# Performance work log

Measured on AMD Instinct MI355X. Metric: run time of the kernel, lower is better.

The kernel has to match this reference:

```python
import jax, jax.numpy as jnp
import numpy as np
import math

N = 50000      # nodes
E = 800000     # edges (avg degree 16)
T = 4          # time steps
F = 64         # feature dim (in = hidden = out)
MAX_LEN = 200  # positional encoding table length
EPS = 1e-5     # BatchNorm eps


def _make_pe(time_dim, max_len):
    pe = np.zeros((max_len, time_dim), dtype=np.float32)
    position = np.arange(max_len, dtype=np.float32)[:, None]
    div_term = np.exp(np.arange(0, time_dim, 2, dtype=np.float32) * (-math.log(10000.0) / time_dim))
    pe[:, 0::2] = np.sin(position * div_term)
    pe[:, 1::2] = np.cos(position * div_term)
    return jnp.asarray(pe)


def setup_inputs() -> dict:
    key = jax.random.key(0)
    ks = jax.random.split(key, 10)
    xav = math.sqrt(2.0 / (F + F))  # xavier_normal_ std for square linear
    return {
        "node_features": jax.random.normal(ks[0], (N, T, F), dtype=jnp.float32),
        "edges_weight": jax.random.uniform(ks[1], (T, E), dtype=jnp.float32),
        "identities": jax.random.randint(ks[2], (T,), 0, MAX_LEN),
        "edge_src": jax.random.randint(ks[3], (E,), 0, N),
        "edge_dst": jax.random.randint(ks[4], (E,), 0, N),
        "pe": _make_pe(F, MAX_LEN),
        "W0": jax.random.normal(ks[5], (F, F), dtype=jnp.float32) * xav,
        "W1": jax.random.normal(ks[6], (F, F), dtype=jnp.float32) * xav,
        "g0": jnp.ones((F,), jnp.float32),
        "b0": jnp.zeros((F,), jnp.float32),
        "g1": jnp.ones((F,), jnp.float32),
        "b1": jnp.zeros((F,), jnp.float32),
    }


def _gcn_layer(h, ew, edge_src, edge_dst, W):
    # gather-mul-scatter: msg_e = h[src_e] * w_e ; agg_v = sum_{e: dst=v} msg_e
    msg = h[edge_src] * ew                                   # (E, T, F)
    agg = jax.ops.segment_sum(msg, edge_dst, num_segments=N)  # (N, T, F)
    readout = agg.mean(axis=0)                                # dgl.mean_nodes (single graph) -> (T, F)
    return agg @ W, readout @ W


def _batchnorm(x, gamma, beta):
    # training-mode batch stats over all non-channel dims
    mean = x.mean(axis=(0, 1))
    var = x.var(axis=(0, 1))
    return (x - mean) * jax.lax.rsqrt(var + EPS) * gamma + beta


def reference(node_features, edges_weight, identities, edge_src, edge_dst,
              pe, W0, W1, g0, b0, g1, b1):
    # positional encoding added per time step
    h = node_features + pe[identities]          # (N, T, F)
    ew = edges_weight.T[:, :, None]             # (E, T, 1)
    # layer 0: gcn -> dropout(eval=identity) -> BN -> ReLU
    h, readout = _gcn_layer(h, ew, edge_src, edge_dst, W0)
    h = jax.nn.relu(_batchnorm(h, g0, b0))
    # layer 1 (output layer)
    h, readout = _gcn_layer(h, ew, edge_src, edge_dst, W1)
    h = jax.nn.relu(_batchnorm(h, g1, b1))
    return h, readout
```

## Files before the change

kernel.cpp:

```cpp
#include <hip/hip_runtime.h>

#define TF 256

typedef __attribute__((ext_vector_type(8))) short short8;
typedef __attribute__((ext_vector_type(4))) float f32x4;
typedef __attribute__((ext_vector_type(4))) unsigned int uint4v;
typedef __attribute__((ext_vector_type(2))) unsigned int uint2v;

__device__ inline unsigned short f2bf(float x) {
  unsigned u = __float_as_uint(x);
  u += 0x7fffu + ((u >> 16) & 1u);
  return (unsigned short)(u >> 16);
}
__device__ inline unsigned pack2(unsigned short lo, unsigned short hi) {
  return (unsigned)lo | ((unsigned)hi << 16);
}
__device__ inline float bflo(unsigned u) { return __uint_as_float(u << 16); }
__device__ inline float bfhi(unsigned u) { return __uint_as_float(u & 0xffff0000u); }

__global__ void prep_hist_kernel(const float* __restrict__ x, const float* __restrict__ pe,
                                 const int* __restrict__ ids, uint2v* __restrict__ h0, int n4,
                                 const int* __restrict__ dst, int* __restrict__ indeg, int E) {
  const int gid = blockIdx.x * blockDim.x + threadIdx.x;
  const int stride = gridDim.x * blockDim.x;
  for (int i = gid; i < n4; i += stride) {
    int e0 = (i << 2) & (TF - 1);
    int t = e0 >> 6;
    int f4 = e0 & 63;
    f32x4 v = __builtin_nontemporal_load(&reinterpret_cast<const f32x4*>(x)[i]);
    const f32x4 p = *reinterpret_cast<const f32x4*>(&pe[ids[t] * 64 + f4]);
    uint2v o;
    o.x = pack2(f2bf(v.x + p.x), f2bf(v.y + p.y));
    o.y = pack2(f2bf(v.z + p.z), f2bf(v.w + p.w));
    h0[i] = o;
  }
  for (int e = gid; e < E; e += stride) {
    atomicAdd(&indeg[__builtin_nontemporal_load(&dst[e])], 1);
  }
}

__global__ __launch_bounds__(1024) void scan_part1(const int* __restrict__ indeg,
                                                   int* __restrict__ partials, int n) {
  __shared__ int wsum[16];
  const int tid = threadIdx.x;
  const int lane = tid & 63;
  const int wid = tid >> 6;
  int i = blockIdx.x * 1024 + tid;
  int s = (i < n) ? indeg[i] : 0;
  #pragma unroll
  for (int o = 1; o < 64; o <<= 1) s += __shfl_xor(s, o, 64);
  if (lane == 0) wsum[wid] = s;
  __syncthreads();
  if (tid == 0) {
    int acc = 0;
    #pragma unroll
    for (int w = 0; w < 16; ++w) acc += wsum[w];
    partials[blockIdx.x] = acc;
  }
}

__global__ __launch_bounds__(512) void scan2_wfrag_kernel(
    const int* __restrict__ partials, int* __restrict__ base, int* __restrict__ offsets,
    int nb, int n, const float* __restrict__ W0, const float* __restrict__ W1,
    short* __restrict__ wf0, short* __restrict__ wf1) {
  const int tid = threadIdx.x;
  if (tid < 64) {
    int v = (tid < nb) ? partials[tid] : 0;
    int s = v;
    #pragma unroll
    for (int o = 1; o < 64; o <<= 1) {
      int t = __shfl_up(s, o, 64);
      if (tid >= o) s += t;
    }
    if (tid < nb) base[tid] = s - v;
    if (tid == nb - 1) offsets[n] = s;
  }
  const int frag = tid >> 6, lane = tid & 63;
  const int c = frag >> 1, h = frag & 1;
  const int col = (c << 4) + (lane & 15);
  const int k0 = h * 32 + ((lane >> 4) << 3);
  short* o0 = wf0 + frag * 512 + lane * 8;
  short* o1 = wf1 + frag * 512 + lane * 8;
  #pragma unroll
  for (int i = 0; i < 8; ++i) {
    o0[i] = (short)f2bf(W0[(k0 + i) * 64 + col]);
    o1[i] = (short)f2bf(W1[(k0 + i) * 64 + col]);
  }
}

__global__ __launch_bounds__(1024) void scan_part3(const int* __restrict__ indeg,
                                                   const int* __restrict__ base,
                                                   int* __restrict__ offsets, int n) {
  __shared__ int wsum[16];
  const int tid = threadIdx.x;
  const int lane = tid & 63;
  const int wid = tid >> 6;
  int i = blockIdx.x * 1024 + tid;
  int v = (i < n) ? indeg[i] : 0;
  int s = v;
  #pragma unroll
  for (int o = 1; o < 64; o <<= 1) {
    int t = __shfl_up(s, o, 64);
    if (lane >= o) s += t;
  }
  if (lane == 63) wsum[wid] = s;
  __syncthreads();
  if (tid == 0) {
    int acc = 0;
    #pragma unroll
    for (int w = 0; w < 16; ++w) { int t = wsum[w]; wsum[w] = acc; acc += t; }
  }
  __syncthreads();
  int excl = s - v + wsum[wid] + base[blockIdx.x];
  if (i < n) offsets[i] = excl;
}

__global__ __launch_bounds__(256) void binscatter_kernel(
    const int* __restrict__ src, const int* __restrict__ dst,
    const float* __restrict__ ew, int* __restrict__ gbin_cursor,
    uint4v* __restrict__ tmp, int E, int nbins) {
  __shared__ int hist[256];
  __shared__ int hist2[256];
  __shared__ int basearr[256];
  const int tid = threadIdx.x;
  hist[tid] = 0;
  hist2[tid] = 0;
  __syncthreads();
  const int epb = (E + gridDim.x - 1) / gridDim.x;
  const int beg = blockIdx.x * epb;
  const int end = min(beg + epb, E);
  for (int e = beg + tid; e < end; e += 256)
    atomicAdd(&hist[__builtin_nontemporal_load(&dst[e]) >> 8], 1);
  __syncthreads();
  if (tid < nbins && hist[tid] > 0)
    basearr[tid] = atomicAdd(&gbin_cursor[tid], hist[tid]);
  __syncthreads();
  for (int e = beg + tid; e < end; e += 256) {
    const int d = dst[e];
    const int bin = d >> 8;
    const int idx = atomicAdd(&hist2[bin], 1);
    uint4v ent;
    ent.x = (unsigned)(src[e] << 9);
    ent.y = pack2(f2bf(ew[e]), f2bf(ew[(size_t)E + e]));
    ent.z = pack2(f2bf(ew[2 * (size_t)E + e]), f2bf(ew[3 * (size_t)E + e]));
    ent.w = (unsigned)d;
    const int pos = basearr[bin] + idx;
    if (pos < 8192)
      __builtin_nontemporal_store(ent, &tmp[((size_t)bin << 13) + pos]);
  }
}

__global__ __launch_bounds__(256) void csr_build_kernel(
    const uint4v* __restrict__ tmp, const int* __restrict__ gbin_cursor,
    const int* __restrict__ offsets, uint4v* __restrict__ csr_ent, int n) {
  __shared__ int cur[256];
  const int bin = blockIdx.x;
  const int tid = threadIdx.x;
  const int node = (bin << 8) + tid;
  cur[tid] = (node < n) ? offsets[node] : 0;
  __syncthreads();
  int cnt = gbin_cursor[bin];
  if (cnt > 8192) cnt = 8192;
  const uint4v* bt = tmp + ((size_t)bin << 13);
  for (int i = tid; i < cnt; i += 256) {
    uint4v ent = __builtin_nontemporal_load(&bt[i]);
    const int local = (int)(ent.w & 255u);
    const int pos = atomicAdd(&cur[local], 1);
    ent.w = 0u;
    __builtin_nontemporal_store(ent, &csr_ent[pos]);
  }
}

template <int LAYER>
__global__ __launch_bounds__(256, 6) void fused_agg_mm_kernel(
    const char* __restrict__ h_base, const int* __restrict__ offsets,
    const uint4v* __restrict__ csr_ent, const short* __restrict__ wf,
    const float* __restrict__ red, const float* __restrict__ g,
    const float* __restrict__ b, float inv_count,
    unsigned short* __restrict__ y_bf, float* __restrict__ part, int n_groups) {
  __shared__ unsigned short tile[2][16][72];
  __shared__ float s_sc[64], s_sh[64];
  const int tid = threadIdx.x;
  const int lane = tid & 63;
  const int wid = tid >> 6;
  if (LAYER == 1) {
    if (tid < 64) {
      float sum = red[tid] + red[64 + tid] + red[128 + tid] + red[192 + tid];
      float mean = sum * inv_count;
      float var = red[256 + tid] * inv_count - mean * mean;
      float sc = g[tid] * rsqrtf(var + 1e-5f);
      s_sc[tid] = sc;
      s_sh[tid] = fmaf(-mean, sc, b[tid]);
    }
    __syncthreads();
  }
  const short8 bf0 = *reinterpret_cast<const short8*>(wf + (wid * 2 + 0) * 512 + lane * 8);
  const short8 bf1 = *reinterpret_cast<const short8*>(wf + (wid * 2 + 1) * 512 + lane * 8);

  const int p = lane >> 5;
  const unsigned q = lane & 31;
  const unsigned qb = q << 4;
  const int tw = q >> 3;

  float scv[8], shv[8];
  if (LAYER == 1) {
    const int f0 = (q & 7) << 3;
    #pragma unroll
    for (int j = 0; j < 8; ++j) { scv[j] = s_sc[f0 + j]; shv[j] = s_sh[f0 + j]; }
  }

  f32x4 csum = (f32x4){0.f, 0.f, 0.f, 0.f};
  float ssq = 0.f;
  int buf = 0;

  for (int grp = blockIdx.x; grp < n_groups; grp += gridDim.x) {
    const int v = grp * 4 + wid;
    float acc[8];
    #pragma unroll
    for (int j = 0; j < 8; ++j) acc[j] = 0.f;

    auto wext = [&](uint4v ent) -> float {
      unsigned word = (tw & 2) ? ent.z : ent.y;
      return (tw & 1) ? bfhi(word) : bflo(word);
    };
    auto body = [&](uint4v u, float w) {
      float x[8] = {bflo(u.x), bfhi(u.x), bflo(u.y), bfhi(u.y),
                    bflo(u.z), bfhi(u.z), bflo(u.w), bfhi(u.w)};
      #pragma unroll
      for (int j = 0; j < 8; ++j) {
        float t = x[j];
        if (LAYER == 1) t = fmaxf(0.f, fmaf(t, scv[j], shv[j]));
        acc[j] = fmaf(w, t, acc[j]);
      }
    };

    const int beg = offsets[v];
    const int end = offsets[v + 1];
    int i = beg;
    for (; i + 8 <= end; i += 8) {
      uint4v ent[4];
      #pragma unroll
      for (int c = 0; c < 4; ++c) ent[c] = csr_ent[i + 2 * c + p];
      uint4v row[4];
      #pragma unroll
      for (int c = 0; c < 4; ++c)
        row[c] = *reinterpret_cast<const uint4v*>(h_base + (ent[c].x + qb));
      #pragma unroll
      for (int c = 0; c < 4; ++c) body(row[c], wext(ent[c]));
    }
    for (; i + 2 <= end; i += 2) {
      const uint4v ent = csr_ent[i + p];
      const uint4v row = *reinterpret_cast<const uint4v*>(h_base + (ent.x + qb));
      body(row, wext(ent));
    }
    if (i < end) {
      const uint4v ent = csr_ent[i];
      const uint4v row = *reinterpret_cast<const uint4v*>(h_base + (ent.x + qb));
      body(row, p == 0 ? wext(ent) : 0.f);
    }

    #pragma unroll
    for (int j = 0; j < 8; ++j) acc[j] += __shfl_xor(acc[j], 32, 64);
    if (lane < 32) {
      uint4v o;
      o.x = pack2(f2bf(acc[0]), f2bf(acc[1]));
      o.y = pack2(f2bf(acc[2]), f2bf(acc[3]));
      o.z = pack2(f2bf(acc[4]), f2bf(acc[5]));
      o.w = pack2(f2bf(acc[6]), f2bf(acc[7]));
      *reinterpret_cast<uint4v*>(&tile[buf][wid * 4 + (q >> 3)][(q & 7) * 8]) = o;
    }
    __syncthreads();

    const int r = lane & 15;
    const int k0 = (lane >> 4) << 3;
    const short8 a0 = *reinterpret_cast<const short8*>(&tile[buf][r][k0]);
    const short8 a1 = *reinterpret_cast<const short8*>(&tile[buf][r][k0 + 32]);
    f32x4 dacc = (f32x4){0.f, 0.f, 0.f, 0.f};
    dacc = __builtin_amdgcn_mfma_f32_16x16x32_bf16(a0, bf0, dacc, 0, 0, 0);
    dacc = __builtin_amdgcn_mfma_f32_16x16x32_bf16(a1, bf1, dacc, 0, 0, 0);
    const int gbase = grp * 16 + ((lane >> 4) << 2);
    const int col = (wid << 4) + (lane & 15);
    #pragma unroll
    for (int i2 = 0; i2 < 4; ++i2) {
      const float val = dacc[i2];
      y_bf[(size_t)(gbase + i2) * 64 + col] = f2bf(val);
      csum[i2] += val;
      ssq += val * val;
    }
    buf ^= 1;
  }

  #pragma unroll
  for (int i2 = 0; i2 < 4; ++i2) {
    float vv = csum[i2];
    vv += __shfl_xor(vv, 16, 64);
    vv += __shfl_xor(vv, 32, 64);
    csum[i2] = vv;
  }
  float qq = ssq;
  qq += __shfl_xor(qq, 16, 64);
  qq += __shfl_xor(qq, 32, 64);
  if (lane < 16) {
    #pragma unroll
    for (int i2 = 0; i2 < 4; ++i2)
      part[(size_t)blockIdx.x * 320 + i2 * 64 + (wid << 4) + lane] = csum[i2];
    part[(size_t)blockIdx.x * 320 + 256 + (wid << 4) + lane] = qq;
  }
}

__global__ __launch_bounds__(1024) void reduce_part_kernel(const float* __restrict__ part,
                                                           float* __restrict__ red, int nblk) {
  __shared__ float lds[1024];
  const int tid = threadIdx.x;
  const int col = blockIdx.x * 16 + (tid & 15);
  const int r = tid >> 4;
  float s = 0.f;
  for (int bk = r; bk < nblk; bk += 64) s += part[(size_t)bk * 320 + col];
  lds[tid] = s;
  __syncthreads();
  #pragma unroll
  for (int off = 512; off >= 16; off >>= 1) {
    if (tid < off) lds[tid] += lds[tid + off];
    __syncthreads();
  }
  if (tid < 16) red[col] = lds[tid];
}

__global__ __launch_bounds__(256) void bn_relu_out_kernel(
    const uint4v* __restrict__ yb, const float* __restrict__ red,
    const float* __restrict__ g, const float* __restrict__ b, float inv_count,
    float* __restrict__ out_readout, float invN, f32x4* __restrict__ out, int n8) {
  __shared__ float s_sc[64], s_sh[64];
  const int tid = threadIdx.x;
  if (tid < 64) {
    float sum = red[tid] + red[64 + tid] + red[128 + tid] + red[192 + tid];
    float mean = sum * inv_count;
    float var = red[256 + tid] * inv_count - mean * mean;
    float sc = g[tid] * rsqrtf(var + 1e-5f);
    s_sc[tid] = sc;
    s_sh[tid] = fmaf(-mean, sc, b[tid]);
  }
  __syncthreads();
  if (blockIdx.x == 0) out_readout[tid] = red[tid] * invN;
  const int i = blockIdx.x * 256 + tid;
  if (i >= n8) return;
  const int f0 = (i & 7) << 3;
  uint4v u = __builtin_nontemporal_load(&yb[i]);
  float x[8] = {bflo(u.x), bfhi(u.x), bflo(u.y), bfhi(u.y),
                bflo(u.z), bfhi(u.z), bflo(u.w), bfhi(u.w)};
  f32x4 o0, o1;
  o0.x = fmaxf(0.f, fmaf(x[0], s_sc[f0 + 0], s_sh[f0 + 0]));
  o0.y = fmaxf(0.f, fmaf(x[1], s_sc[f0 + 1], s_sh[f0 + 1]));
  o0.z = fmaxf(0.f, fmaf(x[2], s_sc[f0 + 2], s_sh[f0 + 2]));
  o0.w = fmaxf(0.f, fmaf(x[3], s_sc[f0 + 3], s_sh[f0 + 3]));
  o1.x = fmaxf(0.f, fmaf(x[4], s_sc[f0 + 4], s_sh[f0 + 4]));
  o1.y = fmaxf(0.f, fmaf(x[5], s_sc[f0 + 5], s_sh[f0 + 5]));
  o1.z = fmaxf(0.f, fmaf(x[6], s_sc[f0 + 6], s_sh[f0 + 6]));
  o1.w = fmaxf(0.f, fmaf(x[7], s_sc[f0 + 7], s_sh[f0 + 7]));
  __builtin_nontemporal_store(o0, &out[i * 2 + 0]);
  __builtin_nontemporal_store(o1, &out[i * 2 + 1]);
}

extern "C" void kernel_launch(void* const* d_in, const int* in_sizes, int n_in,
                              void* d_out, int out_size, void* d_ws, size_t ws_size,
                              hipStream_t stream) {
  const float* node_features = (const float*)d_in[0];
  const float* edges_weight  = (const float*)d_in[1];
  const int*   identities    = (const int*)d_in[2];
  const int*   edge_src      = (const int*)d_in[3];
  const int*   edge_dst      = (const int*)d_in[4];
  const float* pe            = (const float*)d_in[5];
  const float* W0            = (const float*)d_in[6];
  const float* W1            = (const float*)d_in[7];
  const float* g0            = (const float*)d_in[8];
  const float* b0            = (const float*)d_in[9];
  const float* g1            = (const float*)d_in[10];
  const float* b1            = (const float*)d_in[11];

  const int T = in_sizes[2];
  const int E = in_sizes[3];
  const int F = in_sizes[8];
  const int N = in_sizes[0] / (T * F);
  const int R = N * T;
  const int nbins = (N + 255) >> 8;

  float* out = (float*)d_out;
  float* out_h = out;
  float* out_readout = out + (size_t)N * T * F;

  char* ws = (char*)d_ws;
  size_t off = 0;
  auto alloc = [&](size_t bytes) -> void* {
    off = (off + 255) & ~(size_t)255;
    void* p = ws + off;
    off += bytes;
    return p;
  };
  int* zeros = (int*)alloc(((size_t)N + 256) * sizeof(int));
  int* indeg = zeros;
  int* gbin_cursor = zeros + N;
  int*    partials = (int*)alloc(64 * sizeof(int));
  int*    base_    = (int*)alloc(64 * sizeof(int));
  int*    offsets  = (int*)alloc(((size_t)N + 1) * sizeof(int));
  uint4v* csr_ent  = (uint4v*)alloc(((size_t)E + 16) * 16);
  uint4v* tmp      = (uint4v*)alloc(((size_t)nbins << 13) * 16);
  unsigned short* h0b  = (unsigned short*)alloc((size_t)N * TF * 2);
  unsigned short* y0b  = (unsigned short*)alloc((size_t)N * TF * 2);
  short* wf0 = (short*)alloc(8 * 512 * sizeof(short));
  short* wf1 = (short*)alloc(8 * 512 * sizeof(short));
  const int FB = 1536;
  float* mm_part = (float*)alloc((size_t)FB * 320 * sizeof(float));
  float* red     = (float*)alloc(320 * sizeof(float));
  (void)ws_size;

  const int nb = (N + 1023) / 1024;
  const float invR = 1.0f / (float)R;
  const int n_groups = N / 4;

  (void)hipMemsetAsync(zeros, 0, ((size_t)N + 256) * sizeof(int), stream);
  hipLaunchKernelGGL(prep_hist_kernel, dim3(2048), dim3(256), 0, stream,
                     node_features, pe, identities, (uint2v*)h0b, (N * TF) / 4,
                     edge_dst, indeg, E);
  hipLaunchKernelGGL(binscatter_kernel, dim3(256), dim3(256), 0, stream,
                     edge_src, edge_dst, edges_weight, gbin_cursor, tmp, E, nbins);
  hipLaunchKernelGGL(scan_part1, dim3(nb), dim3(1024), 0, stream, indeg, partials, N);
  hipLaunchKernelGGL(scan2_wfrag_kernel, dim3(1), dim3(512), 0, stream,
                     partials, base_, offsets, nb, N, W0, W1, wf0, wf1);
  hipLaunchKernelGGL(scan_part3, dim3(nb), dim3(1024), 0, stream, indeg, base_, offsets, N);
  hipLaunchKernelGGL(csr_build_kernel, dim3(nbins), dim3(256), 0, stream,
                     tmp, gbin_cursor, offsets, csr_ent, N);

  hipLaunchKernelGGL((fused_agg_mm_kernel<0>), dim3(FB), dim3(256), 0, stream,
                     (const char*)h0b, offsets, csr_ent, wf0,
                     nullptr, nullptr, nullptr, 0.f, y0b, mm_part, n_groups);
  hipLaunchKernelGGL(reduce_part_kernel, dim3(20), dim3(1024), 0, stream, mm_part, red, FB);

  hipLaunchKernelGGL((fused_agg_mm_kernel<1>), dim3(FB), dim3(256), 0, stream,
                     (const char*)y0b, offsets, csr_ent, wf1,
                     red, g0, b0, invR, h0b , mm_part, n_groups);
  hipLaunchKernelGGL(reduce_part_kernel, dim3(20), dim3(1024), 0, stream, mm_part, red, FB);

  hipLaunchKernelGGL(bn_relu_out_kernel, dim3((R * 8 + 255) / 256), dim3(256), 0, stream,
                     (const uint4v*)h0b, red, g1, b1, invR,
                     out_readout, 1.0f / (float)N, (f32x4*)out_h, R * 8);
}
```

Measured before the change: 285.1 us.

## Derive CSR offsets inside per-bin build, dropping global degree histogram and scans

```diff
diff --git a/kernel.cpp b/kernel.cpp
--- a/kernel.cpp
+++ b/kernel.cpp
@@ -18,10 +18,12 @@
 __device__ inline float bflo(unsigned u) { return __uint_as_float(u << 16); }
 __device__ inline float bfhi(unsigned u) { return __uint_as_float(u & 0xffff0000u); }
 
-__global__ void prep_hist_kernel(const float* __restrict__ x, const float* __restrict__ pe,
-                                 const int* __restrict__ ids, uint2v* __restrict__ h0, int n4,
-                                 const int* __restrict__ dst, int* __restrict__ indeg, int E) {
-  const int gid = blockIdx.x * blockDim.x + threadIdx.x;
+__global__ void prep_kernel(const float* __restrict__ x, const float* __restrict__ pe,
+                            const int* __restrict__ ids, uint2v* __restrict__ h0, int n4,
+                            const float* __restrict__ W0, const float* __restrict__ W1,
+                            short* __restrict__ wf0, short* __restrict__ wf1) {
+  const int tid = threadIdx.x;
+  const int gid = blockIdx.x * blockDim.x + tid;
   const int stride = gridDim.x * blockDim.x;
   for (int i = gid; i < n4; i += stride) {
     int e0 = (i << 2) & (TF - 1);
@@ -34,85 +36,23 @@
     o.y = pack2(f2bf(v.z + p.z), f2bf(v.w + p.w));
     h0[i] = o;
   }
-  for (int e = gid; e < E; e += stride) {
-    atomicAdd(&indeg[__builtin_nontemporal_load(&dst[e])], 1);
-  }
-}
-
-__global__ __launch_bounds__(1024) void scan_part1(const int* __restrict__ indeg,
-                                                   int* __restrict__ partials, int n) {
-  __shared__ int wsum[16];
-  const int tid = threadIdx.x;
-  const int lane = tid & 63;
-  const int wid = tid >> 6;
-  int i = blockIdx.x * 1024 + tid;
-  int s = (i < n) ? indeg[i] : 0;
-  #pragma unroll
-  for (int o = 1; o < 64; o <<= 1) s += __shfl_xor(s, o, 64);
-  if (lane == 0) wsum[wid] = s;
-  __syncthreads();
-  if (tid == 0) {
-    int acc = 0;
-    #pragma unroll
-    for (int w = 0; w < 16; ++w) acc += wsum[w];
-    partials[blockIdx.x] = acc;
-  }
-}
-
-__global__ __launch_bounds__(512) void scan2_wfrag_kernel(
-    const int* __restrict__ partials, int* __restrict__ base, int* __restrict__ offsets,
-    int nb, int n, const float* __restrict__ W0, const float* __restrict__ W1,
-    short* __restrict__ wf0, short* __restrict__ wf1) {
-  const int tid = threadIdx.x;
-  if (tid < 64) {
-    int v = (tid < nb) ? partials[tid] : 0;
-    int s = v;
-    #pragma unroll
-    for (int o = 1; o < 64; o <<= 1) {
-      int t = __shfl_up(s, o, 64);
-      if (tid >= o) s += t;
-    }
-    if (tid < nb) base[tid] = s - v;
-    if (tid == nb - 1) offsets[n] = s;
-  }
-  const int frag = tid >> 6, lane = tid & 63;
-  const int c = frag >> 1, h = frag & 1;
-  const int col = (c << 4) + (lane & 15);
-  const int k0 = h * 32 + ((lane >> 4) << 3);
-  short* o0 = wf0 + frag * 512 + lane * 8;
-  short* o1 = wf1 + frag * 512 + lane * 8;
-  #pragma unroll
-  for (int i = 0; i < 8; ++i) {
-    o0[i] = (short)f2bf(W0[(k0 + i) * 64 + col]);
-    o1[i] = (short)f2bf(W1[(k0 + i) * 64 + col]);
-  }
-}
-
-__global__ __launch_bounds__(1024) void scan_part3(const int* __restrict__ indeg,
-                                                   const int* __restrict__ base,
-                                                   int* __restrict__ offsets, int n) {
-  __shared__ int wsum[16];
-  const int tid = threadIdx.x;
-  const int lane = tid & 63;
-  const int wid = tid >> 6;
-  int i = blockIdx.x * 1024 + tid;
-  int v = (i < n) ? indeg[i] : 0;
-  int s = v;
-  #pragma unroll
-  for (int o = 1; o < 64; o <<= 1) {
-    int t = __shfl_up(s, o, 64);
-    if (lane >= o) s += t;
-  }
-  if (lane == 63) wsum[wid] = s;
-  __syncthreads();
-  if (tid == 0) {
-    int acc = 0;
-    #pragma unroll
-    for (int w = 0; w < 16; ++w) { int t = wsum[w]; wsum[w] = acc; acc += t; }
-  }
-  __syncthreads();
-  int excl = s - v + wsum[wid] + base[blockIdx.x];
-  if (i < n) offsets[i] = excl;
+  if (blockIdx.x == gridDim.x - 1) {
+    const int lane = tid & 63;
+    #pragma unroll
+    for (int fi = 0; fi < 2; ++fi) {
+      const int frag = (tid >> 6) + fi * 4;
+      const int c = frag >> 1, h = frag & 1;
+      const int col = (c << 4) + (lane & 15);
+      const int k0 = h * 32 + ((lane >> 4) << 3);
+      short* o0 = wf0 + frag * 512 + lane * 8;
+      short* o1 = wf1 + frag * 512 + lane * 8;
+      #pragma unroll
+      for (int i = 0; i < 8; ++i) {
+        o0[i] = (short)f2bf(W0[(k0 + i) * 64 + col]);
+        o1[i] = (short)f2bf(W1[(k0 + i) * 64 + col]);
+      }
+    }
+  }
 }
 
 __global__ __launch_bounds__(256) void binscatter_kernel(
@@ -146,28 +86,68 @@
     ent.w = (unsigned)d;
     const int pos = basearr[bin] + idx;
     if (pos < 8192)
-      __builtin_nontemporal_store(ent, &tmp[((size_t)bin << 13) + pos]);
+      tmp[((size_t)bin << 13) + pos] = ent;
   }
 }
 
 __global__ __launch_bounds__(256) void csr_build_kernel(
-    const uint4v* __restrict__ tmp, const int* __restrict__ gbin_cursor,
-    const int* __restrict__ offsets, uint4v* __restrict__ csr_ent, int n) {
-  __shared__ int cur[256];
+    const uint4v* __restrict__ tmp, const int* __restrict__ gbin_counts,
+    int* __restrict__ offsets, uint4v* __restrict__ csr_ent, int n, int nbins) {
+  __shared__ int hist[256];
+  __shared__ int lbase[256];
+  __shared__ int wsum[4];
+  __shared__ int binbase_s;
   const int bin = blockIdx.x;
   const int tid = threadIdx.x;
+  const int lane = tid & 63;
+  const int wid = tid >> 6;
+  hist[tid] = 0;
+
+  int c = (tid < bin) ? gbin_counts[tid] : 0;
+  int s = c;
+  #pragma unroll
+  for (int o = 1; o < 64; o <<= 1) s += __shfl_xor(s, o, 64);
+  if (lane == 0) wsum[wid] = s;
+  __syncthreads();
+  if (tid == 0) binbase_s = wsum[0] + wsum[1] + wsum[2] + wsum[3];
+  __syncthreads();
+  const int binbase = binbase_s;
+
+  const int cnt = min(gbin_counts[bin], 8192);
+  const uint4v* bt = tmp + ((size_t)bin << 13);
+
+  for (int i = tid; i < cnt; i += 256)
+    atomicAdd(&hist[(int)(bt[i].w & 255u)], 1);
+  __syncthreads();
+
+  int v = hist[tid];
+  int sc = v;
+  #pragma unroll
+  for (int o = 1; o < 64; o <<= 1) {
+    int t = __shfl_up(sc, o, 64);
+    if (lane >= o) sc += t;
+  }
+  if (lane == 63) wsum[wid] = sc;
+  __syncthreads();
+  if (tid == 0) {
+    int acc = 0;
+    #pragma unroll
+    for (int w = 0; w < 4; ++w) { int t = wsum[w]; wsum[w] = acc; acc += t; }
+  }
+  __syncthreads();
+  const int excl = sc - v + wsum[wid] + binbase;
+  lbase[tid] = excl;
   const int node = (bin << 8) + tid;
-  cur[tid] = (node < n) ? offsets[node] : 0;
-  __syncthreads();
-  int cnt = gbin_cursor[bin];
-  if (cnt > 8192) cnt = 8192;
-  const uint4v* bt = tmp + ((size_t)bin << 13);
+  if (node < n) offsets[node] = excl;
+  if (node == n - 1) offsets[n] = binbase + cnt;
+  __syncthreads();
+
   for (int i = tid; i < cnt; i += 256) {
-    uint4v ent = __builtin_nontemporal_load(&bt[i]);
+    uint4v ent = bt[i];
     const int local = (int)(ent.w & 255u);
-    const int pos = atomicAdd(&cur[local], 1);
+    const int pos = atomicAdd(&lbase[local], 1);
     ent.w = 0u;
-    __builtin_nontemporal_store(ent, &csr_ent[pos]);
+    csr_ent[pos] = ent;
   }
 }
 
@@ -396,11 +376,7 @@
     off += bytes;
     return p;
   };
-  int* zeros = (int*)alloc(((size_t)N + 256) * sizeof(int));
-  int* indeg = zeros;
-  int* gbin_cursor = zeros + N;
-  int*    partials = (int*)alloc(64 * sizeof(int));
-  int*    base_    = (int*)alloc(64 * sizeof(int));
+  int*    gbin_cursor = (int*)alloc(256 * sizeof(int));
   int*    offsets  = (int*)alloc(((size_t)N + 1) * sizeof(int));
   uint4v* csr_ent  = (uint4v*)alloc(((size_t)E + 16) * 16);
   uint4v* tmp      = (uint4v*)alloc(((size_t)nbins << 13) * 16);
@@ -413,22 +389,17 @@
   float* red     = (float*)alloc(320 * sizeof(float));
   (void)ws_size;
 
-  const int nb = (N + 1023) / 1024;
   const float invR = 1.0f / (float)R;
   const int n_groups = N / 4;
 
-  (void)hipMemsetAsync(zeros, 0, ((size_t)N + 256) * sizeof(int), stream);
-  hipLaunchKernelGGL(prep_hist_kernel, dim3(2048), dim3(256), 0, stream,
+  (void)hipMemsetAsync(gbin_cursor, 0, 256 * sizeof(int), stream);
+  hipLaunchKernelGGL(binscatter_kernel, dim3(512), dim3(256), 0, stream,
+                     edge_src, edge_dst, edges_weight, gbin_cursor, tmp, E, nbins);
+  hipLaunchKernelGGL(csr_build_kernel, dim3(nbins), dim3(256), 0, stream,
+                     tmp, gbin_cursor, offsets, csr_ent, N, nbins);
+  hipLaunchKernelGGL(prep_kernel, dim3(2048), dim3(256), 0, stream,
                      node_features, pe, identities, (uint2v*)h0b, (N * TF) / 4,
-                     edge_dst, indeg, E);
-  hipLaunchKernelGGL(binscatter_kernel, dim3(256), dim3(256), 0, stream,
-                     edge_src, edge_dst, edges_weight, gbin_cursor, tmp, E, nbins);
-  hipLaunchKernelGGL(scan_part1, dim3(nb), dim3(1024), 0, stream, indeg, partials, N);
-  hipLaunchKernelGGL(scan2_wfrag_kernel, dim3(1), dim3(512), 0, stream,
-                     partials, base_, offsets, nb, N, W0, W1, wf0, wf1);
-  hipLaunchKernelGGL(scan_part3, dim3(nb), dim3(1024), 0, stream, indeg, base_, offsets, N);
-  hipLaunchKernelGGL(csr_build_kernel, dim3(nbins), dim3(256), 0, stream,
-                     tmp, gbin_cursor, offsets, csr_ent, N);
+                     W0, W1, wf0, wf1);
 
   hipLaunchKernelGGL((fused_agg_mm_kernel<0>), dim3(FB), dim3(256), 0, stream,
                      (const char*)h0b, offsets, csr_ent, wf0,
```

After: 231.4 us. 1.23x faster.
